# Kernel tuning notes

Measured on AMD Instinct MI355X. Metric: run time of the kernel, lower is better.

Reference implementation:

```python
import jax, jax.numpy as jnp
import numpy as np

N, M, DIST, HEADS, D, C, DFFN = 16384, 16, 2, 8, 256, 64, 512
DH = D // HEADS
GRID = 128
BLOCK = 2048  # mirrors torch batch_size loop in find_neighboring_voxels_optimized
EPS = 1e-5


def _neighbors(coords_f, src, m, dist):
    """Blockwise Manhattan-distance topk neighbor gather.
    coords_f: (N,3) float voxel coords; src: (N,D) features.
    Returns (N, m, D) neighbor features, zero-filled where fewer than m in range."""
    n = coords_f.shape[0]
    qblocks = coords_f.reshape(-1, BLOCK, 3)

    def one_block(cb):
        # (BLOCK, N) Manhattan distances
        d = jnp.abs(cb[:, None, :] - coords_f[None, :, :]).sum(-1)
        d = jnp.where(d <= dist, d, jnp.inf)
        vals, idx = jax.lax.top_k(-d, m)          # nearest m (self first: dist 0)
        valid = (vals > -jnp.inf)[..., None]
        return jnp.where(valid, src[idx], jnp.zeros((), src.dtype))

    return jax.lax.map(one_block, qblocks).reshape(n, m, src.shape[-1])


def _layernorm(x, g, b):
    mu = x.mean(-1, keepdims=True)
    var = ((x - mu) ** 2).mean(-1, keepdims=True)
    return (x - mu) * jax.lax.rsqrt(var + EPS) * g + b


def setup_inputs() -> dict:
    key = jax.random.key(0)
    ks = jax.random.split(key, 32)
    p = lambda i, shape, s: jax.random.normal(ks[i], shape, dtype=jnp.float32) * s
    z = lambda shape: jnp.zeros(shape, dtype=jnp.float32)
    o = lambda shape: jnp.ones(shape, dtype=jnp.float32)
    return {
        "coords": jax.random.randint(ks[0], (N, 3), 0, GRID, dtype=jnp.int32),
        "features": jax.random.normal(ks[1], (N, C), dtype=jnp.float32),
        "pe_w1": p(2, (3, D // 2), 0.5), "pe_b1": z((D // 2,)),
        "pe_w2": p(3, (D // 2, D), 0.08), "pe_b2": z((D,)),
        "proj_w": p(4, (C, D), 0.12), "proj_b": z((D,)),
        "wq": p(5, (D, D), 0.06), "bq": z((D,)),
        "wk": p(6, (D, D), 0.06), "bk": z((D,)),
        "wv": p(7, (D, D), 0.06), "bv": z((D,)),
        "wo": p(8, (D, D), 0.06), "bo": z((D,)),
        "ffn_w1": p(9, (D, DFFN), 0.06), "ffn_b1": z((DFFN,)),
        "ffn_w2": p(10, (DFFN, D), 0.04), "ffn_b2": z((D,)),
        "ln_g": o((D,)), "ln_b": z((D,)),
        "fus_w1": p(11, (D, C), 0.06), "fus_b1": z((C,)),
        "fus_w2": p(12, (2 * C, C), 0.09), "fus_b2": z((C,)),
        "bn_g": o((C,)), "bn_b": z((C,)),
    }


def reference(coords, features, pe_w1, pe_b1, pe_w2, pe_b2, proj_w, proj_b,
              wq, bq, wk, bk, wv, bv, wo, bo,
              ffn_w1, ffn_b1, ffn_w2, ffn_b2, ln_g, ln_b,
              fus_w1, fus_b1, fus_w2, fus_b2, bn_g, bn_b):
    coords_f = coords.astype(jnp.float32)
    # dynamic learnable positional encoding on normalized coords
    xn = coords_f / (GRID - 1)
    pe = jax.nn.relu(xn @ pe_w1 + pe_b1) @ pe_w2 + pe_b2
    src = features @ proj_w + proj_b + pe                       # (N, D)

    nf = _neighbors(coords_f, src, M, DIST)                     # (N, M, D)
    query = nf[:, 0, :]                                         # (N, D) self-feature

    # multihead attention: query len 1, key len M, batch N
    q = (query @ wq + bq).reshape(N, HEADS, DH)
    k = (nf @ wk + bk).reshape(N, M, HEADS, DH)
    v = (nf @ wv + bv).reshape(N, M, HEADS, DH)
    scores = jnp.einsum('nhd,nmhd->nhm', q, k) / jnp.sqrt(jnp.float32(DH))
    attn = jax.nn.softmax(scores, axis=-1)
    ao = jnp.einsum('nhm,nmhd->nhd', attn, v).reshape(N, D) @ wo + bo  # (N, D)

    # FFN with residual + LayerNorm (dropout=0 / eval)
    h = jax.nn.relu(ao @ ffn_w1 + ffn_b1) @ ffn_w2 + ffn_b2
    y = _layernorm(ao + h, ln_g, ln_b)                          # (N, D)

    # EnhancedFusion: project, concat, linear, BatchNorm1d (batch stats), ReLU
    t = y @ fus_w1 + fus_b1                                     # (N, C)
    f = jnp.concatenate([features, t], axis=1) @ fus_w2 + fus_b2
    mu = f.mean(0)
    var = ((f - mu) ** 2).mean(0)
    f = (f - mu) * jax.lax.rsqrt(var + EPS) * bn_g + bn_b
    return jax.nn.relu(f)                                       # (N, C)
```

## Files before the change

### kernel.cpp

```cpp
#include <hip/hip_runtime.h>
#include <stdint.h>

typedef unsigned short u16;
typedef unsigned int   u32;
typedef __attribute__((ext_vector_type(8))) short short8;
typedef __attribute__((ext_vector_type(4))) float f32x4;

static constexpr int kN = 16384;
static constexpr float kEPS = 1e-5f;

__device__ __forceinline__ u16 f2bf(float x) {
  u32 u = __float_as_uint(x);
  u32 r = (u + 0x7fffu + ((u >> 16) & 1u)) >> 16;
  return (u16)r;
}
__device__ __forceinline__ float bf2f(u16 x) {
  return __uint_as_float(((u32)x) << 16);
}
__device__ __forceinline__ void ldbf8(const u16* p, float* o) {
  uint4 v = *(const uint4*)p;
  o[0] = __uint_as_float(v.x << 16);  o[1] = __uint_as_float(v.x & 0xffff0000u);
  o[2] = __uint_as_float(v.y << 16);  o[3] = __uint_as_float(v.y & 0xffff0000u);
  o[4] = __uint_as_float(v.z << 16);  o[5] = __uint_as_float(v.z & 0xffff0000u);
  o[6] = __uint_as_float(v.w << 16);  o[7] = __uint_as_float(v.w & 0xffff0000u);
}
__device__ __forceinline__ void gll16(const u16* g, u16* l) {
  __builtin_amdgcn_global_load_lds(
      (const __attribute__((address_space(1))) void*)g,
      (__attribute__((address_space(3))) void*)l, 16, 0, 0);
}

struct WSet {
  const float* s[8]; u16* d[8];
  int K[8]; int N[8]; int dstride[8]; int coff[8];
};

__global__ __launch_bounds__(256) void k_setup(WSet ws,
                                               u32* __restrict__ zero_area,
                                               const float* __restrict__ proj_b,
                                               const float* __restrict__ pe_b2,
                                               float* __restrict__ pbc,
                                               const float* __restrict__ uw1,
                                               const float* __restrict__ ub1,
                                               const float* __restrict__ uw2,
                                               const float* __restrict__ ub2,
                                               u16* __restrict__ W2f,
                                               float* __restrict__ bbf,
                                               const int* __restrict__ coords,
                                               const float* __restrict__ feats,
                                               const float* __restrict__ pw1,
                                               const float* __restrict__ pb1,
                                               u16* __restrict__ A1,
                                               u16* __restrict__ A2) {
  int w = blockIdx.y;
  if (w == 8) {
    int idx = blockIdx.x * 256 + threadIdx.x;
    if (idx < 33088) zero_area[idx] = 0u;
    return;
  }
  if (w == 9) {
    int bx = blockIdx.x;
    if (bx == 0) {
      pbc[threadIdx.x] = proj_b[threadIdx.x] + pe_b2[threadIdx.x];
    } else if (bx < 65) {
      int n = bx - 1;
      int k = threadIdx.x;
      float s = 0.f;
      for (int j = 0; j < 64; j++) s += uw1[k * 64 + j] * uw2[(64 + j) * 64 + n];
      W2f[n * 320 + k] = f2bf(s);
      if (k < 64) W2f[n * 320 + 256 + k] = f2bf(uw2[k * 64 + n]);
      if (k == 0) {
        float b = ub2[n];
        for (int j = 0; j < 64; j++) b += ub1[j] * uw2[(64 + j) * 64 + n];
        bbf[n] = b;
      }
    }
    return;
  }
  if (w == 10) {
    int r0 = blockIdx.x * 32;
#pragma unroll
    for (int s = 0; s < 3; s++) {
      int j = threadIdx.x + s * 256;
      int row = j / 24, seg = j % 24;
      int n = r0 + row;
      u16 o[8];
      if (seg < 8) {
        const float* fp = feats + (size_t)n * 64 + seg * 8;
        float4 a = *(const float4*)fp;
        float4 b = *(const float4*)(fp + 4);
        o[0] = f2bf(a.x); o[1] = f2bf(a.y); o[2] = f2bf(a.z); o[3] = f2bf(a.w);
        o[4] = f2bf(b.x); o[5] = f2bf(b.y); o[6] = f2bf(b.z); o[7] = f2bf(b.w);
        *(uint4*)(A2 + (size_t)n * 320 + 256 + seg * 8) = *(uint4*)o;
      } else {
        int jj0 = (seg - 8) * 8;
        float x0 = (float)coords[n * 3 + 0] * (1.f / 127.f);
        float x1 = (float)coords[n * 3 + 1] * (1.f / 127.f);
        float x2 = (float)coords[n * 3 + 2] * (1.f / 127.f);
#pragma unroll
        for (int u = 0; u < 8; u++) {
          int jj = jj0 + u;
          float hv = pb1[jj] + x0 * pw1[jj] + x1 * pw1[128 + jj] + x2 * pw1[256 + jj];
          o[u] = f2bf(fmaxf(hv, 0.f));
        }
      }
      *(uint4*)(A1 + (size_t)n * 192 + seg * 8) = *(uint4*)o;
    }
    return;
  }
  const float* S = ws.s[w]; u16* D = ws.d[w];
  int K = ws.K[w], N = ws.N[w], ds = ws.dstride[w], co = ws.coff[w];
  int ntx = N >> 5, tiles = ntx * (K >> 5);
  int t = blockIdx.x;
  if (t >= tiles) return;
  int n0 = (t % ntx) * 32, k0 = (t / ntx) * 32;
  __shared__ float st[32][33];
  int tr = threadIdx.x >> 3, tc4 = (threadIdx.x & 7) * 4;
  float4 v = *(const float4*)(S + (size_t)(k0 + tr) * N + n0 + tc4);
  st[tc4 + 0][tr] = v.x; st[tc4 + 1][tr] = v.y;
  st[tc4 + 2][tr] = v.z; st[tc4 + 3][tr] = v.w;
  __syncthreads();
  u16 o4[4];
  o4[0] = f2bf(st[tr][tc4 + 0]); o4[1] = f2bf(st[tr][tc4 + 1]);
  o4[2] = f2bf(st[tr][tc4 + 2]); o4[3] = f2bf(st[tr][tc4 + 3]);
  *(uint2*)(D + (size_t)(n0 + tr) * ds + co + k0 + tc4) = *(uint2*)o4;
}


__global__ __launch_bounds__(256) void k_hist(const int* __restrict__ coords,
                                              u32* __restrict__ cnt) {
  int n = blockIdx.x * 256 + threadIdx.x;
  int c = coords[n * 3] * 128 + coords[n * 3 + 1];
  atomicAdd(&cnt[c], 1u);
}

__global__ __launch_bounds__(256) void k_scan(const u32* __restrict__ cnt,
                                              u32* __restrict__ startb) {
  __shared__ u32 tots[256];
  int t = threadIdx.x;
  int base = t * 64;
  u32 s = 0;
  for (int i = 0; i < 64; i++) s += cnt[base + i];
  tots[t] = s;
  __syncthreads();
  if (t == 0) {
    u32 run = 0;
    for (int i = 0; i < 256; i++) { u32 v = tots[i]; tots[i] = run; run += v; }
  }
  __syncthreads();
  u32 run = tots[t];
  for (int i = 0; i < 64; i++) { startb[base + i] = run; run += cnt[base + i]; }
}

__global__ __launch_bounds__(256) void k_scatter(const int* __restrict__ coords,
                                                 const u32* __restrict__ startb,
                                                 u32* __restrict__ cursor,
                                                 u32* __restrict__ pts) {
  int n = blockIdx.x * 256 + threadIdx.x;
  int x = coords[n * 3], y = coords[n * 3 + 1], z = coords[n * 3 + 2];
  int c = x * 128 + y;
  u32 slot = atomicAdd(&cursor[c], 1u);
  pts[startb[c] + slot] = ((u32)z << 14) | (u32)n;
}

__global__ __launch_bounds__(256) void k_select(const int* __restrict__ coords,
                                                const u32* __restrict__ startb,
                                                const u32* __restrict__ cnt,
                                                const u32* __restrict__ pts,
                                                int* __restrict__ idxo) {
  int n = blockIdx.x * 256 + threadIdx.x;
  int x = coords[n * 3], y = coords[n * 3 + 1], z = coords[n * 3 + 2];
  u32 best[16];
#pragma unroll
  for (int j = 0; j < 16; j++) best[j] = 0xFFFFFFFFu;
  const int dxs[13] = {0, -1, 1, 0, 0, -2, 2, 0, 0, -1, -1, 1, 1};
  const int dys[13] = {0, 0, 0, -1, 1, 0, 0, -2, 2, -1, 1, -1, 1};
  const int dbs[13] = {0, 1, 1, 1, 1, 2, 2, 2, 2, 2, 2, 2, 2};
#pragma unroll
  for (int t = 0; t < 13; t++) {
    int xx = x + dxs[t], yy = y + dys[t];
    if (xx < 0 || xx > 127 || yy < 0 || yy > 127) continue;
    int c = xx * 128 + yy;
    u32 s0 = startb[c], e0 = s0 + cnt[c];
    for (u32 i = s0; i < e0; ++i) {
      u32 p = pts[i];
      int zq = (int)(p >> 14);
      int id = (int)(p & 16383u);
      int az = z - zq; az = az < 0 ? -az : az;
      int dd = dbs[t] + az;
      u32 key = (dd <= 2) ? (((u32)dd << 14) | (u32)id) : 0xFFFFFFFFu;
#pragma unroll
      for (int j = 0; j < 16; j++) {
        u32 lo = min(best[j], key);
        u32 hi = max(best[j], key);
        best[j] = lo; key = hi;
      }
    }
  }
#pragma unroll
  for (int j = 0; j < 16; j++)
    idxo[n * 16 + j] = (best[j] == 0xFFFFFFFFu) ? -1 : (int)(best[j] & 16383u);
}

template <int ACT, int OUTBF, int ADD>
__global__ __launch_bounds__(256) void k_mfma_gemm(
    const u16* __restrict__ A, const u16* __restrict__ WT,
    const float* __restrict__ bias,
    void* __restrict__ Cout,
    const u16* __restrict__ Addp,
    int M, int K, int N) {
  __shared__ __align__(16) u16 As[64 * 32];
  __shared__ __align__(16) u16 Bs[64 * 32];
  const int tid = threadIdx.x;
  const int wave = tid >> 6, lane = tid & 63;
  const int bm = blockIdx.y * 64, bn = blockIdx.x * 64;
  const int wr = (wave >> 1) * 32, wc = (wave & 1) * 32;
  const int g = wave * 64 + lane;
  const int grow = g >> 2, gko = (g & 3) * 8;
  const int fr = lane & 15, fk = (lane >> 4) * 8, rq = (lane >> 4) * 4;

  f32x4 acc[2][2];
#pragma unroll
  for (int i = 0; i < 2; i++)
#pragma unroll
    for (int j = 0; j < 2; j++)
#pragma unroll
      for (int r = 0; r < 4; r++) acc[i][j][r] = 0.f;

  for (int k0 = 0; k0 < K; k0 += 32) {
    gll16(A + (size_t)(bm + grow) * K + k0 + gko, As + g * 8);
    gll16(WT + (size_t)(bn + grow) * K + k0 + gko, Bs + g * 8);
    __syncthreads();
    short8 af[2], bg[2];
#pragma unroll
    for (int i = 0; i < 2; i++)
      af[i] = *(const short8*)&As[(wr + i * 16 + fr) * 32 + fk];
#pragma unroll
    for (int j = 0; j < 2; j++)
      bg[j] = *(const short8*)&Bs[(wc + j * 16 + fr) * 32 + fk];
#pragma unroll
    for (int i = 0; i < 2; i++)
#pragma unroll
      for (int j = 0; j < 2; j++)
        acc[i][j] = __builtin_amdgcn_mfma_f32_16x16x32_bf16(af[i], bg[j], acc[i][j], 0, 0, 0);
    __syncthreads();
  }

#pragma unroll
  for (int j = 0; j < 2; j++) {
    int cc = bn + wc + j * 16 + fr;
    float bval = bias ? bias[cc] : 0.f;
#pragma unroll
    for (int i = 0; i < 2; i++) {
      int rbase = bm + wr + i * 16 + rq;
#pragma unroll
      for (int r = 0; r < 4; r++) {
        float v = acc[i][j][r] + bval;
        size_t o = (size_t)(rbase + r) * N + cc;
        if (ADD) v += bf2f(Addp[o]);
        if (ACT) v = fmaxf(v, 0.f);
        if (OUTBF) ((u16*)Cout)[o] = f2bf(v);
        else       ((float*)Cout)[o] = v;
      }
    }
  }
}

__global__ __launch_bounds__(256) void k_attn(const u16* __restrict__ QKV,
                                              const u32* __restrict__ pts,
                                              const int* __restrict__ idx,
                                              const float* __restrict__ bq,
                                              const float* __restrict__ bk,
                                              const float* __restrict__ bv,
                                              u16* __restrict__ outp) {
  int gid = blockIdx.x * 256 + threadIdx.x;
  int n = (int)(pts[gid >> 3] & 16383u), h = gid & 7;
  const int* ip = idx + n * 16;
  const int hb = h * 32;
  float q[32];
  {
    int i0 = ip[0];
    const u16* qp = QKV + (size_t)i0 * 768 + hb;
#pragma unroll
    for (int j = 0; j < 32; j += 8) ldbf8(qp + j, &q[j]);
#pragma unroll
    for (int j = 0; j < 32; j++) q[j] += bq[hb + j];
  }
  float qbk = 0.f;
#pragma unroll
  for (int j = 0; j < 32; j++) qbk += q[j] * bk[hb + j];
  float s[16]; int ii[16];
#pragma unroll
  for (int m = 0; m < 16; m++) {
    int i = ip[m]; ii[m] = i;
    float d = qbk;
    if (i >= 0) {
      const u16* kp = QKV + (size_t)i * 768 + 256 + hb;
      float kv[32];
#pragma unroll
      for (int j = 0; j < 32; j += 8) ldbf8(kp + j, &kv[j]);
#pragma unroll
      for (int j = 0; j < 32; j++) d += q[j] * kv[j];
    }
    s[m] = d * 0.17677669529663689f;
  }
  float mx = s[0];
#pragma unroll
  for (int m = 1; m < 16; m++) mx = fmaxf(mx, s[m]);
  float sum = 0.f;
#pragma unroll
  for (int m = 0; m < 16; m++) { s[m] = __expf(s[m] - mx); sum += s[m]; }
  float inv = 1.f / sum;
  float o[32];
#pragma unroll
  for (int j = 0; j < 32; j++) o[j] = 0.f;
#pragma unroll
  for (int m = 0; m < 16; m++) {
    if (ii[m] >= 0) {
      const u16* vp = QKV + (size_t)ii[m] * 768 + 512 + hb;
      float vv[32];
#pragma unroll
      for (int j = 0; j < 32; j += 8) ldbf8(vp + j, &vv[j]);
#pragma unroll
      for (int j = 0; j < 32; j++) o[j] += s[m] * vv[j];
    }
  }
  u16* op = outp + (size_t)n * 256 + hb;
#pragma unroll
  for (int j = 0; j < 32; j += 8) {
    u16 tmp[8];
#pragma unroll
    for (int jj = 0; jj < 8; jj++) tmp[jj] = f2bf(o[j + jj] * inv + bv[hb + j + jj]);
    *(uint4*)(op + j) = *(uint4*)tmp;
  }
}

__global__ __launch_bounds__(256) void k_ln(const u16* __restrict__ xx,
                                            const float* __restrict__ g,
                                            const float* __restrict__ b,
                                            u16* __restrict__ A2) {
  int row = blockIdx.x * 4 + (threadIdx.x >> 6);
  int lane = threadIdx.x & 63;
  uint2 raw = *(const uint2*)(xx + (size_t)row * 256 + lane * 4);
  float x0 = __uint_as_float(raw.x << 16), x1 = __uint_as_float(raw.x & 0xffff0000u);
  float x2 = __uint_as_float(raw.y << 16), x3 = __uint_as_float(raw.y & 0xffff0000u);
  float sm = x0 + x1 + x2 + x3;
#pragma unroll
  for (int off = 1; off < 64; off <<= 1) sm += __shfl_xor(sm, off);
  float mu = sm * (1.f / 256.f);
  float d0 = x0 - mu, d1 = x1 - mu, d2 = x2 - mu, d3 = x3 - mu;
  float sq = d0 * d0 + d1 * d1 + d2 * d2 + d3 * d3;
#pragma unroll
  for (int off = 1; off < 64; off <<= 1) sq += __shfl_xor(sq, off);
  float rstd = rsqrtf(sq * (1.f / 256.f) + kEPS);
  float4 gv = *(const float4*)(g + lane * 4);
  float4 bv4 = *(const float4*)(b + lane * 4);
  u16 o[4];
  o[0] = f2bf(d0 * rstd * gv.x + bv4.x); o[1] = f2bf(d1 * rstd * gv.y + bv4.y);
  o[2] = f2bf(d2 * rstd * gv.z + bv4.z); o[3] = f2bf(d3 * rstd * gv.w + bv4.w);
  *(uint2*)(A2 + (size_t)row * 320 + lane * 4) = *(uint2*)o;
}

__global__ __launch_bounds__(256) void k_tail(const u16* __restrict__ A2,
                                              const u16* __restrict__ W2f,
                                              const float* __restrict__ bbf,
                                              float* __restrict__ pS,
                                              float* __restrict__ pQ,
                                              u32* __restrict__ arrive,
                                              u32* __restrict__ done,
                                              const float* __restrict__ bng,
                                              const float* __restrict__ bnb,
                                              float* __restrict__ coef,
                                              float* __restrict__ shift,
                                              float* __restrict__ out) {
  __shared__ __align__(16) u16 As[2048];
  __shared__ __align__(16) u16 Bs[2048];
  __shared__ float colS[64][2], colQ[64][2];
  __shared__ u32 lastf;
  const int tid = threadIdx.x;
  const int wave = tid >> 6, lane = tid & 63;
  const int bm = blockIdx.x * 64;
  const int wr = (wave >> 1) * 32, wc = (wave & 1) * 32;
  const int fr = lane & 15, fk = (lane >> 4) * 8, rq = (lane >> 4) * 4;
  const int g = wave * 64 + lane;
  const int grow = g >> 2, gko = (g & 3) * 8;

  f32x4 acc[2][2];
#pragma unroll
  for (int i = 0; i < 2; i++)
#pragma unroll
    for (int j = 0; j < 2; j++)
#pragma unroll
      for (int r = 0; r < 4; r++) acc[i][j][r] = 0.f;
  for (int k0 = 0; k0 < 320; k0 += 32) {
    gll16(A2 + (size_t)(bm + grow) * 320 + k0 + gko, As + g * 8);
    gll16(W2f + (size_t)grow * 320 + k0 + gko, Bs + g * 8);
    __syncthreads();
    short8 af[2], bg[2];
#pragma unroll
    for (int i = 0; i < 2; i++)
      af[i] = *(const short8*)&As[(wr + i * 16 + fr) * 32 + fk];
#pragma unroll
    for (int j = 0; j < 2; j++)
      bg[j] = *(const short8*)&Bs[(wc + j * 16 + fr) * 32 + fk];
#pragma unroll
    for (int i = 0; i < 2; i++)
#pragma unroll
      for (int j = 0; j < 2; j++)
        acc[i][j] = __builtin_amdgcn_mfma_f32_16x16x32_bf16(af[i], bg[j], acc[i][j], 0, 0, 0);
    __syncthreads();
  }
  float cS[2] = {0.f, 0.f}, cQ[2] = {0.f, 0.f};
#pragma unroll
  for (int j = 0; j < 2; j++) {
    int col = wc + j * 16 + fr;
    float bv = bbf[col];
#pragma unroll
    for (int i = 0; i < 2; i++)
#pragma unroll
      for (int r = 0; r < 4; r++) {
        float v = acc[i][j][r] + bv;
        acc[i][j][r] = v;
        cS[j] += v; cQ[j] += v * v;
      }
  }
#pragma unroll
  for (int off = 16; off < 64; off <<= 1) {
#pragma unroll
    for (int j = 0; j < 2; j++) {
      cS[j] += __shfl_xor(cS[j], off);
      cQ[j] += __shfl_xor(cQ[j], off);
    }
  }
  if ((lane >> 4) == 0) {
#pragma unroll
    for (int j = 0; j < 2; j++) {
      colS[wc + j * 16 + fr][wave >> 1] = cS[j];
      colQ[wc + j * 16 + fr][wave >> 1] = cQ[j];
    }
  }
  __syncthreads();
  if (tid < 64) {
    atomicAdd(&pS[tid], colS[tid][0] + colS[tid][1]);
    atomicAdd(&pQ[tid], colQ[tid][0] + colQ[tid][1]);
  }
  __syncthreads();
  if (tid == 0) {
    __threadfence();
    u32 old = __hip_atomic_fetch_add(arrive, 1u, __ATOMIC_ACQ_REL, __HIP_MEMORY_SCOPE_AGENT);
    lastf = (old == 255) ? 1u : 0u;
  }
  __syncthreads();
  if (lastf) {
    if (tid < 64) {
      float S = __hip_atomic_load(&pS[tid], __ATOMIC_ACQUIRE, __HIP_MEMORY_SCOPE_AGENT);
      float Q = __hip_atomic_load(&pQ[tid], __ATOMIC_ACQUIRE, __HIP_MEMORY_SCOPE_AGENT);
      float m = S * (1.f / 16384.f);
      float var = Q * (1.f / 16384.f) - m * m;
      float cf = rsqrtf(var + kEPS) * bng[tid];
      __hip_atomic_store(&coef[tid], cf, __ATOMIC_RELAXED, __HIP_MEMORY_SCOPE_AGENT);
      __hip_atomic_store(&shift[tid], bnb[tid] - m * cf, __ATOMIC_RELAXED, __HIP_MEMORY_SCOPE_AGENT);
    }
    __syncthreads();
    if (tid == 0) {
      __threadfence();
      __hip_atomic_store(done, 1u, __ATOMIC_RELEASE, __HIP_MEMORY_SCOPE_AGENT);
    }
  }
  if (tid == 0) {
    while (__hip_atomic_load(done, __ATOMIC_ACQUIRE, __HIP_MEMORY_SCOPE_AGENT) == 0u) {}
    __threadfence();
  }
  __syncthreads();
#pragma unroll
  for (int j = 0; j < 2; j++) {
    int col = wc + j * 16 + fr;
    float cf = __hip_atomic_load(&coef[col], __ATOMIC_RELAXED, __HIP_MEMORY_SCOPE_AGENT);
    float sh = __hip_atomic_load(&shift[col], __ATOMIC_RELAXED, __HIP_MEMORY_SCOPE_AGENT);
#pragma unroll
    for (int i = 0; i < 2; i++) {
      int rbase = bm + wr + i * 16 + rq;
#pragma unroll
      for (int r = 0; r < 4; r++)
        out[(size_t)(rbase + r) * 64 + col] = fmaxf(acc[i][j][r] * cf + sh, 0.f);
    }
  }
}

extern "C" void kernel_launch(void* const* d_in, const int* in_sizes, int n_in,
                              void* d_out, int out_size, void* d_ws, size_t ws_size,
                              hipStream_t stream) {
  (void)in_sizes; (void)n_in; (void)out_size; (void)ws_size;
  const int*   coords = (const int*)d_in[0];
  const float* feats  = (const float*)d_in[1];
  const float* pe_w1  = (const float*)d_in[2];
  const float* pe_b1  = (const float*)d_in[3];
  const float* pe_w2  = (const float*)d_in[4];
  const float* pe_b2  = (const float*)d_in[5];
  const float* proj_w = (const float*)d_in[6];
  const float* proj_b = (const float*)d_in[7];
  const float* wq  = (const float*)d_in[8];
  const float* bq  = (const float*)d_in[9];
  const float* wk  = (const float*)d_in[10];
  const float* bk  = (const float*)d_in[11];
  const float* wv  = (const float*)d_in[12];
  const float* bv  = (const float*)d_in[13];
  const float* wo  = (const float*)d_in[14];
  const float* bo  = (const float*)d_in[15];
  const float* fw1 = (const float*)d_in[16];
  const float* fb1 = (const float*)d_in[17];
  const float* fw2 = (const float*)d_in[18];
  const float* fb2 = (const float*)d_in[19];
  const float* lng = (const float*)d_in[20];
  const float* lnb = (const float*)d_in[21];
  const float* uw1 = (const float*)d_in[22];
  const float* ub1 = (const float*)d_in[23];
  const float* uw2 = (const float*)d_in[24];
  const float* ub2 = (const float*)d_in[25];
  const float* bng = (const float*)d_in[26];
  const float* bnb = (const float*)d_in[27];
  float* out = (float*)d_out;

  char* Wc = (char*)d_ws;
  const size_t MB = 1u << 20;
  u16*   A1    = (u16*)(Wc + 0 * MB);
  u16*   srcb  = (u16*)(Wc + 6 * MB);
  u16*   QKVb  = (u16*)(Wc + 14 * MB);
  u16*   aoInB = (u16*)(Wc + 38 * MB);
  u16*   aoB   = (u16*)(Wc + 46 * MB);
  u16*   h1B   = (u16*)(Wc + 54 * MB);
  u16*   xBb   = (u16*)(Wc + 70 * MB);
  u16*   A2    = (u16*)(Wc + 78 * MB);

  u16* qkvT  = (u16*)(Wc + 88 * MB);
  u16* woT   = qkvT + 196608;
  u16* fw1T  = woT + 65536;
  u16* fw2T  = fw1T + 131072;
  u16* W1T   = fw2T + 131072;
  u16* W2f   = W1T + 49152;
  float* pbc = (float*)(W2f + 20480);
  float* bbf = pbc + 256;

  u32* Z      = (u32*)(Wc + 90 * MB);
  u32* cnt    = Z;
  u32* cursor = Z + 16384;
  float* pS   = (float*)(Z + 32768);
  float* pQ   = (float*)(Z + 32832);
  u32* arrive = Z + 32897;
  u32* done   = Z + 32898;
  float* coefb = (float*)(Z + 32912);
  float* shb   = coefb + 64;
  u32* startb = Z + 33280;
  u32* pts    = Z + 49664;
  int* idxb   = (int*)(Z + 66048);

  WSet ws;
  ws.s[0] = wq;     ws.d[0] = qkvT;          ws.K[0] = 256; ws.N[0] = 256; ws.dstride[0] = 256; ws.coff[0] = 0;
  ws.s[1] = wk;     ws.d[1] = qkvT + 65536;  ws.K[1] = 256; ws.N[1] = 256; ws.dstride[1] = 256; ws.coff[1] = 0;
  ws.s[2] = wv;     ws.d[2] = qkvT + 131072; ws.K[2] = 256; ws.N[2] = 256; ws.dstride[2] = 256; ws.coff[2] = 0;
  ws.s[3] = wo;     ws.d[3] = woT;           ws.K[3] = 256; ws.N[3] = 256; ws.dstride[3] = 256; ws.coff[3] = 0;
  ws.s[4] = fw1;    ws.d[4] = fw1T;          ws.K[4] = 256; ws.N[4] = 512; ws.dstride[4] = 256; ws.coff[4] = 0;
  ws.s[5] = fw2;    ws.d[5] = fw2T;          ws.K[5] = 512; ws.N[5] = 256; ws.dstride[5] = 512; ws.coff[5] = 0;
  ws.s[6] = proj_w; ws.d[6] = W1T;           ws.K[6] = 64;  ws.N[6] = 256; ws.dstride[6] = 192; ws.coff[6] = 0;
  ws.s[7] = pe_w2;  ws.d[7] = W1T;           ws.K[7] = 128; ws.N[7] = 256; ws.dstride[7] = 192; ws.coff[7] = 64;

  k_setup<<<dim3(512, 11), 256, 0, stream>>>(ws, Z, proj_b, pe_b2, pbc,
                                             uw1, ub1, uw2, ub2, W2f, bbf,
                                             coords, feats, pe_w1, pe_b1, A1, A2);
  k_hist<<<64, 256, 0, stream>>>(coords, cnt);
  k_scan<<<1, 256, 0, stream>>>(cnt, startb);
  k_scatter<<<64, 256, 0, stream>>>(coords, startb, cursor, pts);
  k_select<<<64, 256, 0, stream>>>(coords, startb, cnt, pts, idxb);
  k_mfma_gemm<0, 1, 0><<<dim3(4, 256), 256, 0, stream>>>(A1, W1T, pbc, srcb, nullptr, kN, 192, 256);
  k_mfma_gemm<0, 1, 0><<<dim3(12, 256), 256, 0, stream>>>(srcb, qkvT, nullptr, QKVb, nullptr, kN, 256, 768);
  k_attn<<<512, 256, 0, stream>>>(QKVb, pts, idxb, bq, bk, bv, aoInB);
  k_mfma_gemm<0, 1, 0><<<dim3(4, 256), 256, 0, stream>>>(aoInB, woT, bo, aoB, nullptr, kN, 256, 256);
  k_mfma_gemm<1, 1, 0><<<dim3(8, 256), 256, 0, stream>>>(aoB, fw1T, fb1, h1B, nullptr, kN, 256, 512);
  k_mfma_gemm<0, 1, 1><<<dim3(4, 256), 256, 0, stream>>>(h1B, fw2T, fb2, xBb, aoB, kN, 512, 256);
  k_ln<<<4096, 256, 0, stream>>>(xBb, lng, lnb, A2);
  k_tail<<<256, 256, 0, stream>>>(A2, W2f, bbf, pS, pQ, arrive, done, bng, bnb, coefb, shb, out);
}
```

Measured before the change: 282.7 us.

## Split fused tail kernel into GEMM, BN-finalize, and BN-apply launches

Replaces the single tail kernel, which used a grid-wide spin barrier (arrive/done counters) to compute batch-norm statistics and then apply them, with three kernels. The first does the fusion GEMM, writes the fp32 pre-BN activations to workspace and accumulates column sums. The second computes the per-column scale and shift, and the third applies BN plus ReLU. This removes the in-kernel spin-wait and its dependence on every block being co-resident. In exchange it adds two kernel launches and a 4 MB fp32 round trip through global memory.

```diff
diff --git a/kernel.cpp b/kernel.cpp
--- a/kernel.cpp
+++ b/kernel.cpp
@@ -361,22 +361,15 @@
   *(uint2*)(A2 + (size_t)row * 320 + lane * 4) = *(uint2*)o;
 }
 
-__global__ __launch_bounds__(256) void k_tail(const u16* __restrict__ A2,
-                                              const u16* __restrict__ W2f,
-                                              const float* __restrict__ bbf,
-                                              float* __restrict__ pS,
-                                              float* __restrict__ pQ,
-                                              u32* __restrict__ arrive,
-                                              u32* __restrict__ done,
-                                              const float* __restrict__ bng,
-                                              const float* __restrict__ bnb,
-                                              float* __restrict__ coef,
-                                              float* __restrict__ shift,
-                                              float* __restrict__ out) {
+__global__ __launch_bounds__(256) void k_fgemm(const u16* __restrict__ A2,
+                                               const u16* __restrict__ W2f,
+                                               const float* __restrict__ bbf,
+                                               float* __restrict__ fB,
+                                               float* __restrict__ pS,
+                                               float* __restrict__ pQ) {
   __shared__ __align__(16) u16 As[2048];
   __shared__ __align__(16) u16 Bs[2048];
   __shared__ float colS[64][2], colQ[64][2];
-  __shared__ u32 lastf;
   const int tid = threadIdx.x;
   const int wave = tid >> 6, lane = tid & 63;
   const int bm = blockIdx.x * 64;
@@ -416,13 +409,15 @@
     int col = wc + j * 16 + fr;
     float bv = bbf[col];
 #pragma unroll
-    for (int i = 0; i < 2; i++)
+    for (int i = 0; i < 2; i++) {
+      int rbase = bm + wr + i * 16 + rq;
 #pragma unroll
       for (int r = 0; r < 4; r++) {
         float v = acc[i][j][r] + bv;
-        acc[i][j][r] = v;
+        fB[(size_t)(rbase + r) * 64 + col] = v;
         cS[j] += v; cQ[j] += v * v;
       }
+    }
   }
 #pragma unroll
   for (int off = 16; off < 64; off <<= 1) {
@@ -444,47 +439,38 @@
     atomicAdd(&pS[tid], colS[tid][0] + colS[tid][1]);
     atomicAdd(&pQ[tid], colQ[tid][0] + colQ[tid][1]);
   }
-  __syncthreads();
-  if (tid == 0) {
-    __threadfence();
-    u32 old = __hip_atomic_fetch_add(arrive, 1u, __ATOMIC_ACQ_REL, __HIP_MEMORY_SCOPE_AGENT);
-    lastf = (old == 255) ? 1u : 0u;
-  }
-  __syncthreads();
-  if (lastf) {
-    if (tid < 64) {
-      float S = __hip_atomic_load(&pS[tid], __ATOMIC_ACQUIRE, __HIP_MEMORY_SCOPE_AGENT);
-      float Q = __hip_atomic_load(&pQ[tid], __ATOMIC_ACQUIRE, __HIP_MEMORY_SCOPE_AGENT);
-      float m = S * (1.f / 16384.f);
-      float var = Q * (1.f / 16384.f) - m * m;
-      float cf = rsqrtf(var + kEPS) * bng[tid];
-      __hip_atomic_store(&coef[tid], cf, __ATOMIC_RELAXED, __HIP_MEMORY_SCOPE_AGENT);
-      __hip_atomic_store(&shift[tid], bnb[tid] - m * cf, __ATOMIC_RELAXED, __HIP_MEMORY_SCOPE_AGENT);
-    }
-    __syncthreads();
-    if (tid == 0) {
-      __threadfence();
-      __hip_atomic_store(done, 1u, __ATOMIC_RELEASE, __HIP_MEMORY_SCOPE_AGENT);
-    }
-  }
-  if (tid == 0) {
-    while (__hip_atomic_load(done, __ATOMIC_ACQUIRE, __HIP_MEMORY_SCOPE_AGENT) == 0u) {}
-    __threadfence();
-  }
-  __syncthreads();
-#pragma unroll
-  for (int j = 0; j < 2; j++) {
-    int col = wc + j * 16 + fr;
-    float cf = __hip_atomic_load(&coef[col], __ATOMIC_RELAXED, __HIP_MEMORY_SCOPE_AGENT);
-    float sh = __hip_atomic_load(&shift[col], __ATOMIC_RELAXED, __HIP_MEMORY_SCOPE_AGENT);
-#pragma unroll
-    for (int i = 0; i < 2; i++) {
-      int rbase = bm + wr + i * 16 + rq;
-#pragma unroll
-      for (int r = 0; r < 4; r++)
-        out[(size_t)(rbase + r) * 64 + col] = fmaxf(acc[i][j][r] * cf + sh, 0.f);
-    }
-  }
+}
+
+__global__ __launch_bounds__(64) void k_bnfin(const float* __restrict__ pS,
+                                              const float* __restrict__ pQ,
+                                              const float* __restrict__ g,
+                                              const float* __restrict__ b,
+                                              float* __restrict__ coef,
+                                              float* __restrict__ shift) {
+  int c = threadIdx.x;
+  float S = pS[c], Q = pQ[c];
+  float m = S * (1.f / 16384.f);
+  float var = Q * (1.f / 16384.f) - m * m;
+  float cf = rsqrtf(var + kEPS) * g[c];
+  coef[c] = cf;
+  shift[c] = b[c] - m * cf;
+}
+
+__global__ __launch_bounds__(256) void k_bnapply(const float* __restrict__ f,
+                                                 const float* __restrict__ coef,
+                                                 const float* __restrict__ shift,
+                                                 float* __restrict__ out) {
+  int gid = blockIdx.x * 256 + threadIdx.x;
+  int e = gid * 4, col = e & 63;
+  float4 v = *(const float4*)(f + e);
+  float4 cf = *(const float4*)(coef + col);
+  float4 sh = *(const float4*)(shift + col);
+  float4 o;
+  o.x = fmaxf(v.x * cf.x + sh.x, 0.f);
+  o.y = fmaxf(v.y * cf.y + sh.y, 0.f);
+  o.z = fmaxf(v.z * cf.z + sh.z, 0.f);
+  o.w = fmaxf(v.w * cf.w + sh.w, 0.f);
+  *(float4*)(out + e) = o;
 }
 
 extern "C" void kernel_launch(void* const* d_in, const int* in_sizes, int n_in,
@@ -531,6 +517,7 @@
   u16*   h1B   = (u16*)(Wc + 54 * MB);
   u16*   xBb   = (u16*)(Wc + 70 * MB);
   u16*   A2    = (u16*)(Wc + 78 * MB);
+  float* fB    = (float*)(Wc + 0 * MB);
 
   u16* qkvT  = (u16*)(Wc + 88 * MB);
   u16* woT   = qkvT + 196608;
@@ -546,8 +533,6 @@
   u32* cursor = Z + 16384;
   float* pS   = (float*)(Z + 32768);
   float* pQ   = (float*)(Z + 32832);
-  u32* arrive = Z + 32897;
-  u32* done   = Z + 32898;
   float* coefb = (float*)(Z + 32912);
   float* shb   = coefb + 64;
   u32* startb = Z + 33280;
@@ -578,5 +563,7 @@
   k_mfma_gemm<1, 1, 0><<<dim3(8, 256), 256, 0, stream>>>(aoB, fw1T, fb1, h1B, nullptr, kN, 256, 512);
   k_mfma_gemm<0, 1, 1><<<dim3(4, 256), 256, 0, stream>>>(h1B, fw2T, fb2, xBb, aoB, kN, 512, 256);
   k_ln<<<4096, 256, 0, stream>>>(xBb, lng, lnb, A2);
-  k_tail<<<256, 256, 0, stream>>>(A2, W2f, bbf, pS, pQ, arrive, done, bng, bnb, coefb, shb, out);
-}
+  k_fgemm<<<256, 256, 0, stream>>>(A2, W2f, bbf, fB, pS, pQ);
+  k_bnfin<<<1, 64, 0, stream>>>(pS, pQ, bng, bnb, coefb, shb);
+  k_bnapply<<<1024, 256, 0, stream>>>(fB, coefb, shb, out);
+}
```

Result: faster. 252.3 us (-10.7%).
